# Optimization experiments

Measured on AMD Instinct MI355X. Metric: run time of the kernel, lower is better.

## Reference

```python
import jax, jax.numpy as jnp
import numpy as np
from jax import lax

K = 3      # kernel size
PAD = 1    # padding (stride=1, dilation=1, single offset group)


def _deform_conv2d(x, off, weight, bias):
    # x: [B,C,H,W], off: [B,2*K*K,H,W] (y,x per tap), weight: [O,C,K,K], bias: [O]
    B, C, H, W = x.shape
    KK = K * K
    off = off.reshape(B, KK, 2, H, W)
    off_y, off_x = off[:, :, 0], off[:, :, 1]          # [B,KK,H,W]

    kh = jnp.repeat(jnp.arange(K, dtype=x.dtype), K)   # [KK] tap row offsets
    kw = jnp.tile(jnp.arange(K, dtype=x.dtype), K)     # [KK] tap col offsets
    py = (jnp.arange(H, dtype=x.dtype)[None, None, :, None] - PAD
          + kh[None, :, None, None] + off_y)           # [B,KK,H,W] sample rows
    px = (jnp.arange(W, dtype=x.dtype)[None, None, None, :] - PAD
          + kw[None, :, None, None] + off_x)           # [B,KK,H,W] sample cols

    y0 = jnp.floor(py); x0 = jnp.floor(px)
    wy1 = py - y0; wx1 = px - x0
    wy0 = 1.0 - wy1; wx0 = 1.0 - wx1

    bidx = jnp.arange(B)[:, None, None, None]

    def gather(iy, ix):
        # zero outside the input (torchvision semantics)
        valid = (iy >= 0) & (iy < H) & (ix >= 0) & (ix < W)
        iyc = jnp.clip(iy, 0, H - 1).astype(jnp.int32)
        ixc = jnp.clip(ix, 0, W - 1).astype(jnp.int32)
        v = x[bidx, :, iyc, ixc]                       # [B,KK,H,W,C]
        return v * valid[..., None].astype(x.dtype)

    samp = (gather(y0, x0)           * (wy0 * wx0)[..., None]
            + gather(y0, x0 + 1)     * (wy0 * wx1)[..., None]
            + gather(y0 + 1, x0)     * (wy1 * wx0)[..., None]
            + gather(y0 + 1, x0 + 1) * (wy1 * wx1)[..., None])  # [B,KK,H,W,C]

    w = weight.reshape(weight.shape[0], C, KK)          # [O,C,KK]
    out = jnp.einsum('bkhwc,ock->bohw', samp, w) + bias[None, :, None, None]
    return out


def setup_inputs() -> dict:
    key = jax.random.key(0)
    k1, k2, k3 = jax.random.split(key, 3)
    B, C, O, H, W = 4, 64, 64, 128, 128
    x = jax.random.normal(k1, (B, C, H, W), dtype=jnp.float32)
    offset_w = jax.random.normal(k2, (2 * K * K, C, 3, 3), dtype=jnp.float32) * 0.02
    offset_b = jnp.zeros((2 * K * K,), dtype=jnp.float32)
    weight = jax.random.normal(k3, (O, C, K, K), dtype=jnp.float32) * 0.01
    bias = jnp.zeros((O,), dtype=jnp.float32)
    return {"x": x, "offset_w": offset_w, "offset_b": offset_b,
            "weight": weight, "bias": bias}


def reference(x, offset_w, offset_b, weight, bias):
    # offset-predicting conv (3x3, pad 1)
    off = lax.conv_general_dilated(
        x, offset_w, window_strides=(1, 1), padding='SAME',
        dimension_numbers=('NCHW', 'OIHW', 'NCHW')) + offset_b[None, :, None, None]
    return _deform_conv2d(x, off, weight, bias)
```

## Files before the change

kernel.cpp:

```cpp
#include <hip/hip_runtime.h>
#include <hip/hip_bf16.h>


typedef short short8 __attribute__((ext_vector_type(8)));
typedef float f32x4 __attribute__((ext_vector_type(4)));

#define SROW 36
#define PROW 88

static __device__ inline short bf16s(float f) {
    __hip_bfloat16 h = __float2bfloat16(f);
    return *(short*)&h;
}
static __device__ inline float lo2f(unsigned u) { return __uint_as_float(u << 16); }
static __device__ inline float hi2f(unsigned u) { return __uint_as_float(u & 0xffff0000u); }

__global__ void prep_transpose_kernel(const float* __restrict__ x,
                                      __hip_bfloat16* __restrict__ xBp,
                                      const float* __restrict__ offset_w,
                                      const float* __restrict__ weight,
                                      __hip_bfloat16* __restrict__ Wb,
                                      __hip_bfloat16* __restrict__ OWb)
{
    __shared__ __align__(16) float lds[128 * 65];
    int raw = blockIdx.x;
    int t = threadIdx.x;

    if (raw >= 520) {
        int id = (raw - 520) * 256 + t;
        if (id < 36864) {
            int j    = id & 7;
            int lane = (id >> 3) & 63;
            int id3  = id >> 9;
            int s    = id3 % 18;
            int otile = id3 / 18;
            int n = lane & 15, q = lane >> 4;
            int kap = s * 32 + q * 8 + j;
            int k = kap >> 6, c = kap & 63;
            int o = otile * 16 + n;
            Wb[id] = __float2bfloat16(weight[(o * 64 + c) * 9 + k]);
        }
        int id2 = id - 36864;
        if (id2 >= 0 && id2 < 18432) {
            int j    = id2 & 7;
            int lane = (id2 >> 3) & 63;
            int id3  = id2 >> 9;
            int s    = id3 % 18;
            int ntile = id3 / 18;
            int n = lane & 15, q = lane >> 4;
            int kap = s * 32 + q * 8 + j;
            int k = kap >> 6, c = kap & 63;
            int o = ntile * 16 + n;
            float v = (o < 18) ? offset_w[(o * 64 + c) * 9 + k] : 0.0f;
            OWb[id2] = __float2bfloat16(v);
        }
        return;
    }

    int blk = (raw & 7) * 65 + (raw >> 3);
    int b = blk / 130, r = blk - b * 130;
    unsigned* rowp = (unsigned*)(xBp + (size_t)(b * 130 + r) * 130 * 64);
    if (r == 0 || r == 129) {
        uint4 z = {0u, 0u, 0u, 0u};
        for (int i = 0; i < 5; ++i) {
            int e = i * 256 + t;
            if (e < 1040) ((uint4*)rowp)[e] = z;
        }
        return;
    }
    int h = r - 1;
    const float4* x4 = (const float4*)x;
    size_t base4 = (size_t)b * 262144 + (size_t)h * 32;
#pragma unroll
    for (int i = 0; i < 8; ++i) {
        int idx = i * 256 + t;
        int c = idx >> 5, w4 = idx & 31;
        float4 v = x4[base4 + (size_t)c * 4096 + w4];
        int wb = w4 * 4;
        lds[(wb + 0) * 65 + c] = v.x;
        lds[(wb + 1) * 65 + c] = v.y;
        lds[(wb + 2) * 65 + c] = v.z;
        lds[(wb + 3) * 65 + c] = v.w;
    }
    __syncthreads();
    unsigned* dst = rowp + 32;
    for (int i = 0; i < 16; ++i) {
        int L = i * 256 + t;
        int ww = L >> 5, c2 = L & 31;
        float f0 = lds[ww * 65 + c2 * 2];
        float f1 = lds[ww * 65 + c2 * 2 + 1];
        unsigned pk = ((unsigned)bf16s(f0) & 0xffffu) | ((unsigned)bf16s(f1) << 16);
        dst[L] = pk;
    }
    if (t < 64) {
        int col = (t >> 5) * 129;
        rowp[col * 32 + (t & 31)] = 0u;
    }
}

template<int K0, int K1>
static __device__ inline void sample_taps(const __hip_bfloat16* __restrict__ xb8,
                                          const float* __restrict__ offL,
                                          short* __restrict__ sampB,
                                          int h, int w0, int p, int c8)
{
    constexpr int NT = K1 - K0;
    float wa[NT], wb_[NT], wc[NT], wd[NT];
    uint4 r0[NT], r1[NT], r2[NT], r3[NT];
#pragma unroll
    for (int i = 0; i < NT; ++i) {
        int k = K0 + i;
        float offy = offL[(2 * k) * 16 + p];
        float offx = offL[(2 * k + 1) * 16 + p];
        float py = (float)(h - 1 + (k / 3)) + offy;
        float px = (float)(w0 + p - 1 + (k % 3)) + offx;
        float y0f = floorf(py), x0f = floorf(px);
        float wy1 = py - y0f, wx1 = px - x0f;
        float wy0 = 1.0f - wy1, wx0 = 1.0f - wx1;
        int iy = (int)y0f, ix = (int)x0f;
        int iy0 = min(max(iy, -1), 128);
        int ix0 = min(max(ix, -1), 128);
        int iy1 = min(max(iy + 1, -1), 128);
        int ix1 = min(max(ix + 1, -1), 128);
        int rb0 = iy0 * 130, rb1 = iy1 * 130;
        r0[i] = *(const uint4*)(xb8 + (rb0 + ix0) * 64);
        r1[i] = *(const uint4*)(xb8 + (rb0 + ix1) * 64);
        r2[i] = *(const uint4*)(xb8 + (rb1 + ix0) * 64);
        r3[i] = *(const uint4*)(xb8 + (rb1 + ix1) * 64);
        wa[i] = wy0 * wx0;
        wb_[i] = wy0 * wx1;
        wc[i] = wy1 * wx0;
        wd[i] = wy1 * wx1;
    }
#pragma unroll
    for (int i = 0; i < NT; ++i) {
        int k = K0 + i;
        short8 pk;
#define SAMP1(idx, comp, EXT) { \
            float sv = fmaf(wd[i], EXT(r3[i].comp), fmaf(wc[i], EXT(r2[i].comp), \
                       fmaf(wb_[i], EXT(r1[i].comp), wa[i] * EXT(r0[i].comp)))); \
            pk[idx] = bf16s(sv); }
        SAMP1(0, x, lo2f) SAMP1(1, x, hi2f)
        SAMP1(2, y, lo2f) SAMP1(3, y, hi2f)
        SAMP1(4, z, lo2f) SAMP1(5, z, hi2f)
        SAMP1(6, w, lo2f) SAMP1(7, w, hi2f)
#undef SAMP1
        int s = 2 * k + (c8 >> 2);
        *(short8*)&sampB[(s * 16 + p) * SROW + (c8 & 3) * 8] = pk;
    }
}

__global__ __launch_bounds__(256, 4) void deform_kernel(
    const __hip_bfloat16* __restrict__ xBp,
    const __hip_bfloat16* __restrict__ Wb,
    const __hip_bfloat16* __restrict__ OWb,
    const float* __restrict__ offset_b,
    const float* __restrict__ bias,
    float* __restrict__ out)
{
    __shared__ __align__(16) short sampB[18 * 16 * SROW];
    __shared__ __align__(16) float offL[288];

    int t = threadIdx.x, wv = t >> 6, lane = t & 63;
    int bid = (blockIdx.x & 7) * 512 + (blockIdx.x >> 3);
    int b  = bid >> 10;
    int h  = (bid >> 3) & 127;
    int w0 = (bid & 7) << 4;

    short* patch = sampB;

    {
#pragma unroll
        for (int i = 0; i < 2; ++i) {
            int e = i * 256 + t;
            if (e < 432) {
                int px = e >> 3, part = e & 7;
                int row = px / 18, col = px - row * 18;
                const uint4* src = (const uint4*)(xBp +
                    ((size_t)((b * 130 + h + row) * 130) + w0 + col) * 64 + part * 8);
                *(uint4*)&patch[px * PROW + part * 8] = *src;
            }
        }
    }
    __syncthreads();

    if (wv < 2) {
        int n = lane & 15, q = lane >> 4;
        const short8* Bw = (const short8*)OWb + (wv * 18) * 64 + lane;
        f32x4 acc = {0.f, 0.f, 0.f, 0.f};
#pragma unroll
        for (int s = 0; s < 18; ++s) {
            int k = s >> 1;
            int ky = k / 3, kx = k - ky * 3;
            int pix = ky * 18 + n + kx;
            const short8 a = *(const short8*)&patch[pix * PROW + (s & 1) * 32 + q * 8];
            acc = __builtin_amdgcn_mfma_f32_16x16x32_bf16(a, Bw[s * 64], acc, 0, 0, 0);
        }
        int o = wv * 16 + n;
        if (o < 18) {
            float bo = offset_b[o];
#pragma unroll
            for (int r = 0; r < 4; ++r)
                offL[o * 16 + q * 4 + r] = acc[r] + bo;
        }
    }
    __syncthreads();

    {
        int g8 = lane >> 3, c8 = lane & 7;
        int p = (wv & 1) * 8 + g8;
        const __hip_bfloat16* xb8 = xBp + (size_t)b * (130 * 130 * 64) + c8 * 8 + 131 * 64;
        if (wv < 2) sample_taps<0, 4>(xb8, offL, sampB, h, w0, p, c8);
        else        sample_taps<4, 9>(xb8, offL, sampB, h, w0, p, c8);
    }
    __syncthreads();

    {
        int n = lane & 15, q = lane >> 4;
        int arow = n * SROW + q * 8;
        const short8* BwW = (const short8*)Wb + (wv * 18) * 64 + lane;
        f32x4 acc = {0.f, 0.f, 0.f, 0.f};
#pragma unroll
        for (int s = 0; s < 18; ++s) {
            const short8 a = *(const short8*)&sampB[s * (16 * SROW) + arow];
            acc = __builtin_amdgcn_mfma_f32_16x16x32_bf16(a, BwW[s * 64], acc, 0, 0, 0);
        }
        int o = wv * 16 + n;
        float bo = bias[o];
        float4 st = {acc[0] + bo, acc[1] + bo, acc[2] + bo, acc[3] + bo};
        *(float4*)&out[(((size_t)b * 64 + o) * 128 + h) * 128 + w0 + q * 4] = st;
    }
}

extern "C" void kernel_launch(void* const* d_in, const int* in_sizes, int n_in,
                              void* d_out, int out_size, void* d_ws, size_t ws_size,
                              hipStream_t stream) {
    const float* x        = (const float*)d_in[0];
    const float* offset_w = (const float*)d_in[1];
    const float* offset_b = (const float*)d_in[2];
    const float* weight   = (const float*)d_in[3];
    const float* bias     = (const float*)d_in[4];
    char* ws = (char*)d_ws;
    __hip_bfloat16* xBp = (__hip_bfloat16*)ws;
    __hip_bfloat16* Wb  = (__hip_bfloat16*)(ws + 8652800);
    __hip_bfloat16* OWb = (__hip_bfloat16*)(ws + 8652800 + 73728);
    float* outp = (float*)d_out;

    hipLaunchKernelGGL(prep_transpose_kernel, dim3(736),  dim3(256), 0, stream,
                       x, xBp, offset_w, weight, Wb, OWb);
    hipLaunchKernelGGL(deform_kernel,         dim3(4096), dim3(256), 0, stream,
                       xBp, Wb, OWb, offset_b, bias, outp);
}
```

Baseline: 104.7 us.

## Stage a wider 5-row input band in LDS and gather bilinear samples from it

The per-block input patch grows from 3x18 pixels to a 5x24 band held in shared memory, with clamped loads at the borders. The offset-conv MFMA reads from this band, and the bilinear sampling reads its four corner pixels from LDS whenever they fall inside the band, falling back to global memory otherwise. The aim is to replace scattered global gathers with LDS reads, since offsets are small. In exchange, each block uses more LDS and loads more data up front, which may lower occupancy, and the sampling path gains a branch.

New measurement: 128.5 us. 1.23x slower.

```diff
diff --git a/kernel.cpp b/kernel.cpp
--- a/kernel.cpp
+++ b/kernel.cpp
@@ -6,7 +6,8 @@
 typedef float f32x4 __attribute__((ext_vector_type(4)));
 
 #define SROW 36
-#define PROW 88
+#define CSTR 68
+#define RSTR (24 * CSTR)
 
 static __device__ inline short bf16s(float f) {
     __hip_bfloat16 h = __float2bfloat16(f);
@@ -99,7 +100,8 @@
 }
 
 template<int K0, int K1>
-static __device__ inline void sample_taps(const __hip_bfloat16* __restrict__ xb8,
+static __device__ inline void sample_taps(const short* __restrict__ band,
+                                          const __hip_bfloat16* __restrict__ xb8,
                                           const float* __restrict__ offL,
                                           short* __restrict__ sampB,
                                           int h, int w0, int p, int c8)
@@ -122,15 +124,26 @@
         int ix0 = min(max(ix, -1), 128);
         int iy1 = min(max(iy + 1, -1), 128);
         int ix1 = min(max(ix + 1, -1), 128);
-        int rb0 = iy0 * 130, rb1 = iy1 * 130;
-        r0[i] = *(const uint4*)(xb8 + (rb0 + ix0) * 64);
-        r1[i] = *(const uint4*)(xb8 + (rb0 + ix1) * 64);
-        r2[i] = *(const uint4*)(xb8 + (rb1 + ix0) * 64);
-        r3[i] = *(const uint4*)(xb8 + (rb1 + ix1) * 64);
         wa[i] = wy0 * wx0;
         wb_[i] = wy0 * wx1;
         wc[i] = wy1 * wx0;
         wd[i] = wy1 * wx1;
+        int j0  = iy0 - h + 2,  j1  = iy1 - h + 2;
+        int jx0 = ix0 - w0 + 3, jx1 = ix1 - w0 + 3;
+        if ((j0 >= 0) && (j1 <= 4) && (jx0 >= 0) && (jx1 <= 23)) {
+            const short* b0 = band + j0 * RSTR + c8 * 8;
+            const short* b1 = band + j1 * RSTR + c8 * 8;
+            r0[i] = *(const uint4*)(b0 + jx0 * CSTR);
+            r1[i] = *(const uint4*)(b0 + jx1 * CSTR);
+            r2[i] = *(const uint4*)(b1 + jx0 * CSTR);
+            r3[i] = *(const uint4*)(b1 + jx1 * CSTR);
+        } else {
+            int rb0 = iy0 * 130, rb1 = iy1 * 130;
+            r0[i] = *(const uint4*)(xb8 + (rb0 + ix0) * 64);
+            r1[i] = *(const uint4*)(xb8 + (rb0 + ix1) * 64);
+            r2[i] = *(const uint4*)(xb8 + (rb1 + ix0) * 64);
+            r3[i] = *(const uint4*)(xb8 + (rb1 + ix1) * 64);
+        }
     }
 #pragma unroll
     for (int i = 0; i < NT; ++i) {
@@ -158,6 +171,7 @@
     const float* __restrict__ bias,
     float* __restrict__ out)
 {
+    __shared__ __align__(16) short band[5 * RSTR];
     __shared__ __align__(16) short sampB[18 * 16 * SROW];
     __shared__ __align__(16) float offL[288];
 
@@ -167,19 +181,17 @@
     int h  = (bid >> 3) & 127;
     int w0 = (bid & 7) << 4;
 
-    short* patch = sampB;
-
-    {
-#pragma unroll
-        for (int i = 0; i < 2; ++i) {
-            int e = i * 256 + t;
-            if (e < 432) {
-                int px = e >> 3, part = e & 7;
-                int row = px / 18, col = px - row * 18;
-                const uint4* src = (const uint4*)(xBp +
-                    ((size_t)((b * 130 + h + row) * 130) + w0 + col) * 64 + part * 8);
-                *(uint4*)&patch[px * PROW + part * 8] = *src;
-            }
+#pragma unroll
+    for (int i = 0; i < 4; ++i) {
+        int e = i * 256 + t;
+        if (e < 960) {
+            int px = e >> 3, part = e & 7;
+            int j = px / 24, jx = px - j * 24;
+            int prow = min(max(h - 1 + j, 0), 129);
+            int pcol = min(max(w0 - 2 + jx, 0), 129);
+            const uint4* src = (const uint4*)(xBp +
+                ((size_t)(b * 130 + prow) * 130 + pcol) * 64 + part * 8);
+            *(uint4*)&band[j * RSTR + jx * CSTR + part * 8] = *src;
         }
     }
     __syncthreads();
@@ -192,8 +204,8 @@
         for (int s = 0; s < 18; ++s) {
             int k = s >> 1;
             int ky = k / 3, kx = k - ky * 3;
-            int pix = ky * 18 + n + kx;
-            const short8 a = *(const short8*)&patch[pix * PROW + (s & 1) * 32 + q * 8];
+            const short8 a = *(const short8*)&band[(ky + 1) * RSTR + (n + kx + 2) * CSTR
+                                                   + (s & 1) * 32 + q * 8];
             acc = __builtin_amdgcn_mfma_f32_16x16x32_bf16(a, Bw[s * 64], acc, 0, 0, 0);
         }
         int o = wv * 16 + n;
@@ -210,8 +222,8 @@
         int g8 = lane >> 3, c8 = lane & 7;
         int p = (wv & 1) * 8 + g8;
         const __hip_bfloat16* xb8 = xBp + (size_t)b * (130 * 130 * 64) + c8 * 8 + 131 * 64;
-        if (wv < 2) sample_taps<0, 4>(xb8, offL, sampB, h, w0, p, c8);
-        else        sample_taps<4, 9>(xb8, offL, sampB, h, w0, p, c8);
+        if (wv < 2) sample_taps<0, 4>(band, xb8, offL, sampB, h, w0, p, c8);
+        else        sample_taps<4, 9>(band, xb8, offL, sampB, h, w0, p, c8);
     }
     __syncthreads();
 
```
